# Performance work log

Hardware: AMD Instinct MI355X
Metric: run time of the kernel (lower is better)

## Reference

```python
import jax, jax.numpy as jnp
import numpy as np

K = 10
A_JAC = 0.5
B_JAC = 0.5
N_NODES = 100000
N_EDGES = 1600000
IN_CH, HID, OUT_CH = 256, 64, 32
NUM_LAYERS = 2


def setup_inputs() -> dict:
    key = jax.random.key(0)
    k1, k2, k3, k4, k5, k6 = jax.random.split(key, 6)
    x = jax.random.normal(k1, (N_NODES, IN_CH), dtype=jnp.float32)
    edge_index = jax.random.randint(k2, (2, N_EDGES), 0, N_NODES, dtype=jnp.int64)
    W1 = jax.random.normal(k3, (IN_CH, HID), dtype=jnp.float32) / np.sqrt(IN_CH)
    b1 = jnp.zeros((HID,), dtype=jnp.float32)
    coeffs = jnp.ones((NUM_LAYERS, K + 1), dtype=jnp.float32) / (K + 1)
    W2 = jax.random.normal(k4, (HID, OUT_CH), dtype=jnp.float32) / np.sqrt(HID)
    b2 = jnp.zeros((OUT_CH,), dtype=jnp.float32)
    return {"x": x, "edge_index": edge_index, "W1": W1, "b1": b1,
            "coeffs": coeffs, "W2": W2, "b2": b2}


def _build_norm(edge_index, num_nodes):
    # add self loops (as PyG add_self_loops does)
    loops = jnp.arange(num_nodes, dtype=edge_index.dtype)
    row = jnp.concatenate([edge_index[0], loops])
    col = jnp.concatenate([edge_index[1], loops])
    deg = jax.ops.segment_sum(jnp.ones_like(col, dtype=jnp.float32), col,
                              num_segments=num_nodes)
    dinv = jnp.where(deg > 0, deg ** -0.5, 0.0)
    norm = dinv[row] * dinv[col]  # [E + N]
    return row, col, norm


def _propagate(h, row, col, norm, num_nodes):
    # out[i] = sum_{e: col[e]=i} norm[e] * h[row[e]]
    return jax.ops.segment_sum(norm[:, None] * h[row], col, num_segments=num_nodes)


def _jacobi_conv(h, row, col, norm, c, num_nodes):
    a, b = A_JAC, B_JAC
    Tx0 = h
    out = c[0] * Tx0
    Tx1 = _propagate(h, row, col, norm, num_nodes)
    out = out + c[1] * Tx1
    for k in range(2, K + 1):
        n = k - 1
        A_n = (2 * n + a + b + 1) * (2 * n + a + b + 2) / (2 * (n + 1) * (n + a + b + 1))
        B_n = (a ** 2 - b ** 2) * (2 * n + a + b + 1) / (2 * (n + 1) * (n + a + b + 1) * (2 * n + a + b))
        C_n = (n + a) * (n + b) * (2 * n + a + b + 2) / ((n + 1) * (n + a + b + 1) * (2 * n + a + b))
        Tx2 = A_n * _propagate(Tx1, row, col, norm, num_nodes) + B_n * Tx1 - C_n * Tx0
        out = out + c[k] * Tx2
        Tx0, Tx1 = Tx1, Tx2
    return out


def reference(x, edge_index, W1, b1, coeffs, W2, b2):
    num_nodes = x.shape[0]
    row, col, norm = _build_norm(edge_index, num_nodes)
    h = jax.nn.relu(x @ W1 + b1)
    for l in range(NUM_LAYERS):
        h = jax.nn.relu(_jacobi_conv(h, row, col, norm, coeffs[l], num_nodes))
    return h @ W2 + b2
```

## Files before the change

kernel.cpp:

```cpp
#include <hip/hip_runtime.h>
#include <hip/hip_fp16.h>

#define NN 100000
#define NE 1600000
#define KORD 10
#define HID 64

#define NBUK ((NN + 255) / 256)
#define BCAP 8192
#define EPB  (NE / 256)

typedef _Float16 half8v __attribute__((ext_vector_type(8)));
typedef _Float16 half4v __attribute__((ext_vector_type(4)));
typedef float float4v __attribute__((ext_vector_type(4)));

__device__ __forceinline__ float2 up2(unsigned u) {
    __half2 hh = *(__half2*)&u;
    return __half22float2(hh);
}
__device__ __forceinline__ unsigned pk2(float a, float b) {
    __half2 hh = __floats2half2_rn(a, b);
    return *(unsigned*)&hh;
}

__global__ __launch_bounds__(512) void k_zero(int* __restrict__ gcnt,
                                              int* __restrict__ dhist) {
    int t = threadIdx.x;
    if (t < NBUK) gcnt[t] = 0;
    if (t < 64) dhist[t] = 0;
}

__global__ __launch_bounds__(1024) void k_binA(const int* __restrict__ ei,
                                               int* __restrict__ gcnt,
                                               unsigned* __restrict__ staged) {
    __shared__ int lh[NBUK];
    __shared__ int lcur[NBUK];
    int t = threadIdx.x;
    int ebeg = blockIdx.x * EPB;
    int eend = min(ebeg + EPB, NE);
    for (int i = t; i < NBUK; i += 1024) lh[i] = 0;
    __syncthreads();
    for (int e = ebeg + t; e < eend; e += 1024)
        atomicAdd(&lh[ei[NE + e] >> 8], 1);
    __syncthreads();
    for (int i = t; i < NBUK; i += 1024)
        lcur[i] = lh[i] ? atomicAdd(&gcnt[i], lh[i]) : 0;
    __syncthreads();
    for (int e = ebeg + t; e < eend; e += 1024) {
        int r = ei[e], c = ei[NE + e];
        int bkt = c >> 8;
        int slot = atomicAdd(&lcur[bkt], 1);
        if (slot < BCAP)
            staged[(size_t)bkt * BCAP + slot] = ((unsigned)(c & 255) << 24) | (unsigned)r;
    }
}

__global__ __launch_bounds__(512) void k_bscan(const int* __restrict__ gcnt,
                                               int* __restrict__ bbase,
                                               int* __restrict__ cursor) {
    __shared__ int tmp[512];
    int t = threadIdx.x;
    int v = (t < NBUK) ? gcnt[t] : 0;
    tmp[t] = v;
    __syncthreads();
    int x = v;
    for (int off = 1; off < 512; off <<= 1) {
        int y = (t >= off) ? tmp[t - off] : 0;
        __syncthreads();
        x += y;
        tmp[t] = x;
        __syncthreads();
    }
    if (t < NBUK) bbase[t] = x - v;
    if (t == 0) cursor[NN] = NE;
}

__global__ __launch_bounds__(512) void k_binB(const unsigned* __restrict__ staged,
                                              const int* __restrict__ gcnt,
                                              const int* __restrict__ bbase,
                                              int* __restrict__ cursor,
                                              int* __restrict__ cnt,
                                              float* __restrict__ dinv,
                                              int* __restrict__ csr) {
    __shared__ unsigned lrec[BCAP];
    __shared__ int lcnt[256], lcur[256], ltmp[256];
    int b = blockIdx.x, t = threadIdx.x;
    int count = min(gcnt[b], BCAP);
    int base = bbase[b];
    if (t < 256) lcnt[t] = 0;
    __syncthreads();
    for (int i = t; i < count; i += 512) {
        unsigned rec = staged[(size_t)b * BCAP + i];
        lrec[i] = rec;
        atomicAdd(&lcnt[rec >> 24], 1);
    }
    __syncthreads();
    int v = 0, x = 0;
    if (t < 256) { v = lcnt[t]; ltmp[t] = v; }
    __syncthreads();
    x = v;
    for (int off = 1; off < 256; off <<= 1) {
        int y = (t < 256 && t >= off) ? ltmp[t - off] : 0;
        __syncthreads();
        if (t < 256) { x += y; ltmp[t] = x; }
        __syncthreads();
    }
    if (t < 256) {
        int excl = x - v;
        lcur[t] = base + excl;
        int node = b * 256 + t;
        if (node < NN) {
            cursor[node] = base + excl;
            cnt[node] = v;
            dinv[node] = rsqrtf((float)(v + 1));
        }
    }
    __syncthreads();
    for (int i = t; i < count; i += 512) {
        unsigned rec = lrec[i];
        int pos = atomicAdd(&lcur[rec >> 24], 1);
        csr[pos] = (int)(rec & 0xFFFFFFu);
    }
}

__global__ __launch_bounds__(256) void k_dhist(const int* __restrict__ cnt,
                                               int* __restrict__ dhist) {
    __shared__ int lh[64];
    int t = threadIdx.x;
    if (t < 64) lh[t] = 0;
    __syncthreads();
    int i = blockIdx.x * 256 + t;
    if (i < NN) atomicAdd(&lh[min(cnt[i], 63)], 1);
    __syncthreads();
    if (t < 64 && lh[t]) atomicAdd(&dhist[t], lh[t]);
}

__global__ void k_dscan(int* __restrict__ dhist) {
    __shared__ int tmp[64];
    int t = threadIdx.x;
    int v = dhist[t];
    tmp[t] = v;
    __syncthreads();
    int x = v;
    for (int off = 1; off < 64; off <<= 1) {
        int y = (t >= off) ? tmp[t - off] : 0;
        __syncthreads();
        x += y;
        tmp[t] = x;
        __syncthreads();
    }
    dhist[t] = x - v;
}

__global__ __launch_bounds__(256) void k_dperm(const int* __restrict__ cnt,
                                               int* __restrict__ dhist,
                                               int* __restrict__ perm) {
    __shared__ int lh[64], lb[64];
    int t = threadIdx.x;
    if (t < 64) lh[t] = 0;
    __syncthreads();
    int i = blockIdx.x * 256 + t;
    int b = 0, my = 0;
    if (i < NN) { b = min(cnt[i], 63); my = atomicAdd(&lh[b], 1); }
    __syncthreads();
    if (t < 64) lb[t] = lh[t] ? atomicAdd(&dhist[t], lh[t]) : 0;
    __syncthreads();
    if (i < NN) perm[lb[b] + my] = i;
}

__global__ __launch_bounds__(256) void k_zrow(__half* __restrict__ a, __half* __restrict__ b,
                                              __half* __restrict__ c, __half* __restrict__ d) {
    int t = threadIdx.x;
    __half z = __float2half(0.f);
    size_t base = (size_t)NN * HID;
    if (t < 64)       a[base + t] = z;
    else if (t < 128) b[base + (t - 64)] = z;
    else if (t < 192) c[base + (t - 128)] = z;
    else              d[base + (t - 192)] = z;
}

__global__ __launch_bounds__(256) void k_prepw1(const float* __restrict__ W1,
                                                _Float16* __restrict__ W1T) {
    int f = blockIdx.x * 256 + threadIdx.x;
    int n = f >> 8, k = f & 255;
    W1T[f] = (_Float16)W1[k * 64 + n];
}

#define G1K 128
#define G1S 136
__global__ __launch_bounds__(256) void k_gemm1(const float* __restrict__ x,
                                               const _Float16* __restrict__ W1T,
                                               const float* __restrict__ b1,
                                               const float* __restrict__ dinv,
                                               __half* __restrict__ h) {
    __shared__ _Float16 A_lds[64 * G1S];
    __shared__ _Float16 B_lds[64 * G1S];
    int t = threadIdx.x;
    int wave = t >> 6, lane = t & 63;
    int quad = lane >> 4, m16 = lane & 15;
    int row0 = blockIdx.x * 64;

    float4v acc[4];
#pragma unroll
    for (int n4 = 0; n4 < 4; ++n4) acc[n4] = (float4v){0.f, 0.f, 0.f, 0.f};

    for (int c = 0; c < 2; ++c) {
        int k0 = c * G1K;
#pragma unroll
        for (int i = 0; i < 8; ++i) {
            int f = i * 256 + t;
            int r = f >> 5, c4 = f & 31;
            int grow = row0 + r;
            float4 v = (grow < NN) ? *(const float4*)&x[(size_t)grow * 256 + k0 + c4 * 4]
                                   : make_float4(0.f, 0.f, 0.f, 0.f);
            half4v hv = {(_Float16)v.x, (_Float16)v.y, (_Float16)v.z, (_Float16)v.w};
            *(half4v*)&A_lds[r * G1S + c4 * 4] = hv;
        }
#pragma unroll
        for (int i = 0; i < 4; ++i) {
            int f = i * 256 + t;
            int n = f >> 4, k8 = f & 15;
            *(half8v*)&B_lds[n * G1S + k8 * 8] =
                *(const half8v*)&W1T[n * 256 + k0 + k8 * 8];
        }
        __syncthreads();

#pragma unroll
        for (int s = 0; s < 4; ++s) {
            half8v af = *(const half8v*)&A_lds[(wave * 16 + m16) * G1S + s * 32 + quad * 8];
#pragma unroll
            for (int n4 = 0; n4 < 4; ++n4) {
                half8v bf = *(const half8v*)&B_lds[(n4 * 16 + m16) * G1S + s * 32 + quad * 8];
                acc[n4] = __builtin_amdgcn_mfma_f32_16x16x32_f16(af, bf, acc[n4], 0, 0, 0);
            }
        }
        __syncthreads();
    }

    float bv[4];
#pragma unroll
    for (int n4 = 0; n4 < 4; ++n4) bv[n4] = b1[n4 * 16 + m16];
#pragma unroll
    for (int r = 0; r < 4; ++r) {
        int grow = row0 + wave * 16 + quad * 4 + r;
        if (grow >= NN) continue;
        float dv = dinv[grow];
#pragma unroll
        for (int n4 = 0; n4 < 4; ++n4) {
            float v = dv * fmaxf(acc[n4][r] + bv[n4], 0.f);
            h[(size_t)grow * 64 + n4 * 16 + m16] = __float2half(v);
        }
    }
}

__global__ __launch_bounds__(256) void k_prop(const int* __restrict__ cursor,
                                              const int* __restrict__ csr,
                                              const int* __restrict__ perm,
                                              const __half* __restrict__ src,
                                              const __half* __restrict__ t0,
                                              const float* __restrict__ dinv,
                                              __half* __restrict__ dst,
                                              __half* __restrict__ acc,
                                              __half* __restrict__ hout,
                                              float An, float Bn, float Cn,
                                              const float* __restrict__ coeffs,
                                              int cbase, int kidx, int init,
                                              int finalize, int unscale) {
    int slot = ((blockIdx.x * 256 + threadIdx.x) >> 6) * 8 + ((threadIdx.x & 63) >> 3);
    int ch8 = (threadIdx.x & 7) * 8;
    bool valid = slot < NN;
    int node = valid ? perm[slot] : 0;
    int beg = valid ? cursor[node] : 0;
    int end = valid ? cursor[node + 1] : 0;

    int len = end - beg;
    int q = len >> 2;
    int j0 = beg,          e0 = beg + q;
    int j1 = e0,           e1 = beg + 2 * q;
    int j2 = e1,           e2 = beg + 3 * q;
    int j3 = e2,           e3 = end;

    float p[8];
#pragma unroll
    for (int i = 0; i < 8; ++i) p[i] = 0.f;

    while (__any(j3 < e3)) {
        int a0 = (j0 < e0) ? j0 : 0;
        int a1 = (j1 < e1) ? j1 : 0;
        int a2 = (j2 < e2) ? j2 : 0;
        int a3 = (j3 < e3) ? j3 : 0;
        int v0 = csr[a0], v1 = csr[a1], v2 = csr[a2], v3 = csr[a3];
        int r0 = (j0 < e0) ? v0 : NN;
        int r1 = (j1 < e1) ? v1 : NN;
        int r2 = (j2 < e2) ? v2 : NN;
        int r3 = (j3 < e3) ? v3 : NN;
        uint4 u0 = *(const uint4*)&src[(size_t)r0 * HID + ch8];
        uint4 u1 = *(const uint4*)&src[(size_t)r1 * HID + ch8];
        uint4 u2 = *(const uint4*)&src[(size_t)r2 * HID + ch8];
        uint4 u3 = *(const uint4*)&src[(size_t)r3 * HID + ch8];
        {
            float2 f0 = up2(u0.x), f1 = up2(u0.y), f2 = up2(u0.z), f3 = up2(u0.w);
            p[0] += f0.x; p[1] += f0.y; p[2] += f1.x; p[3] += f1.y;
            p[4] += f2.x; p[5] += f2.y; p[6] += f3.x; p[7] += f3.y;
        }
        {
            float2 f0 = up2(u1.x), f1 = up2(u1.y), f2 = up2(u1.z), f3 = up2(u1.w);
            p[0] += f0.x; p[1] += f0.y; p[2] += f1.x; p[3] += f1.y;
            p[4] += f2.x; p[5] += f2.y; p[6] += f3.x; p[7] += f3.y;
        }
        {
            float2 f0 = up2(u2.x), f1 = up2(u2.y), f2 = up2(u2.z), f3 = up2(u2.w);
            p[0] += f0.x; p[1] += f0.y; p[2] += f1.x; p[3] += f1.y;
            p[4] += f2.x; p[5] += f2.y; p[6] += f3.x; p[7] += f3.y;
        }
        {
            float2 f0 = up2(u3.x), f1 = up2(u3.y), f2 = up2(u3.z), f3 = up2(u3.w);
            p[0] += f0.x; p[1] += f0.y; p[2] += f1.x; p[3] += f1.y;
            p[4] += f2.x; p[5] += f2.y; p[6] += f3.x; p[7] += f3.y;
        }
        ++j0; ++j1; ++j2; ++j3;
    }

    if (!valid) return;
    size_t idx = (size_t)node * HID + ch8;
    float dv = dinv[node];
    float dv2 = dv * dv;

    uint4 sr = *(const uint4*)&src[idx];
    float2 s01 = up2(sr.x), s23 = up2(sr.y), s45 = up2(sr.z), s67 = up2(sr.w);
    float sv[8] = {s01.x, s01.y, s23.x, s23.y, s45.x, s45.y, s67.x, s67.y};

    uint4 tr = *(const uint4*)&t0[idx];
    float2 t01 = up2(tr.x), t23 = up2(tr.y), t45 = up2(tr.z), t67 = up2(tr.w);
    float tv[8] = {t01.x, t01.y, t23.x, t23.y, t45.x, t45.y, t67.x, t67.y};

    float v[8];
#pragma unroll
    for (int i = 0; i < 8; ++i)
        v[i] = An * dv2 * (p[i] + sv[i]) + Bn * sv[i] - Cn * tv[i];

    if (!finalize) {
        uint4 o;
        o.x = pk2(v[0], v[1]); o.y = pk2(v[2], v[3]);
        o.z = pk2(v[4], v[5]); o.w = pk2(v[6], v[7]);
        *(uint4*)&dst[idx] = o;
    }

    float ck = coeffs[cbase + kidx];
    float av[8];
    if (init) {
        float c0 = coeffs[cbase];
#pragma unroll
        for (int i = 0; i < 8; ++i) av[i] = c0 * sv[i];
    } else {
        uint4 ar = *(const uint4*)&acc[idx];
        float2 a01 = up2(ar.x), a23 = up2(ar.y), a45 = up2(ar.z), a67 = up2(ar.w);
        av[0] = a01.x; av[1] = a01.y; av[2] = a23.x; av[3] = a23.y;
        av[4] = a45.x; av[5] = a45.y; av[6] = a67.x; av[7] = a67.y;
    }
#pragma unroll
    for (int i = 0; i < 8; ++i) av[i] += ck * v[i];

    uint4 o;
    if (finalize) {
        float s = unscale ? (1.0f / dv) : 1.0f;
        o.x = pk2(s * fmaxf(av[0], 0.f), s * fmaxf(av[1], 0.f));
        o.y = pk2(s * fmaxf(av[2], 0.f), s * fmaxf(av[3], 0.f));
        o.z = pk2(s * fmaxf(av[4], 0.f), s * fmaxf(av[5], 0.f));
        o.w = pk2(s * fmaxf(av[6], 0.f), s * fmaxf(av[7], 0.f));
        *(uint4*)&hout[idx] = o;
    } else {
        o.x = pk2(av[0], av[1]); o.y = pk2(av[2], av[3]);
        o.z = pk2(av[4], av[5]); o.w = pk2(av[6], av[7]);
        *(uint4*)&acc[idx] = o;
    }
}

__global__ __launch_bounds__(256) void k_gemm2(const __half* __restrict__ h,
                                               const float* __restrict__ W2,
                                               const float* __restrict__ b2,
                                               float* __restrict__ out) {
    __shared__ float W2s[64 * 32];
    __shared__ float b2s[32];
    int t = threadIdx.x;
    for (int i = t * 4; i < 64 * 32; i += 256 * 4)
        *(float4*)&W2s[i] = *(const float4*)&W2[i];
    if (t < 32) b2s[t] = b2[t];
    __syncthreads();

    int gid = blockIdx.x * 256 + t;
    int row = gid >> 3;
    int c4 = (t & 7) * 4;
    if (row >= NN) return;
    const __half* hr = h + (size_t)row * 64;
    float4 acc = *(const float4*)&b2s[c4];
#pragma unroll
    for (int k8 = 0; k8 < 8; ++k8) {
        uint4 raw = *(const uint4*)&hr[k8 * 8];
        float2 a01 = up2(raw.x), a23 = up2(raw.y), a45 = up2(raw.z), a67 = up2(raw.w);
        float a[8] = {a01.x, a01.y, a23.x, a23.y, a45.x, a45.y, a67.x, a67.y};
#pragma unroll
        for (int j = 0; j < 8; ++j) {
            float4 w = *(const float4*)&W2s[(k8 * 8 + j) * 32 + c4];
            acc.x += a[j] * w.x;
            acc.y += a[j] * w.y;
            acc.z += a[j] * w.z;
            acc.w += a[j] * w.w;
        }
    }
    *(float4*)&out[(size_t)row * 32 + c4] = acc;
}

extern "C" void kernel_launch(void* const* d_in, const int* in_sizes, int n_in,
                              void* d_out, int out_size, void* d_ws, size_t ws_size,
                              hipStream_t stream) {
    const float* x      = (const float*)d_in[0];
    const int*   ei     = (const int*)d_in[1];
    const float* W1     = (const float*)d_in[2];
    const float* b1     = (const float*)d_in[3];
    const float* coeffs = (const float*)d_in[4];
    const float* W2     = (const float*)d_in[5];
    const float* b2     = (const float*)d_in[6];
    float* out = (float*)d_out;

    char* ws = (char*)d_ws;
    size_t off = 0;
    auto alloc = [&](size_t bytes) { void* p = ws + off; off += (bytes + 255) & ~(size_t)255; return p; };
    int*      cnt    = (int*)alloc(NN * 4);
    int*      cursor = (int*)alloc((NN + 1) * 4);
    float*    dinv   = (float*)alloc(NN * 4);
    int*      csr    = (int*)alloc((size_t)NE * 4);
    int*      dhist  = (int*)alloc(64 * 4);
    int*      perm   = (int*)alloc(NN * 4);
    int*      gcnt   = (int*)alloc(NBUK * 4);
    int*      bbase  = (int*)alloc(NBUK * 4);
    unsigned* staged = (unsigned*)alloc((size_t)NBUK * BCAP * 4);
    _Float16* W1T    = (_Float16*)alloc(256 * 64 * 2);
    __half*   h16    = (__half*)alloc((size_t)(NN + 1) * HID * 2);
    __half*   bufA   = (__half*)alloc((size_t)(NN + 1) * HID * 2);
    __half*   bufB   = (__half*)alloc((size_t)(NN + 1) * HID * 2);
    __half*   bufC   = (__half*)alloc((size_t)(NN + 1) * HID * 2);
    __half*   accb   = (__half*)alloc((size_t)NN * HID * 2);

    const int BN = (NN + 255) / 256;
    const int BP = (NN + 31) / 32;

    k_zero<<<1, 512, 0, stream>>>(gcnt, dhist);
    k_binA<<<256, 1024, 0, stream>>>(ei, gcnt, staged);
    k_bscan<<<1, 512, 0, stream>>>(gcnt, bbase, cursor);
    k_binB<<<NBUK, 512, 0, stream>>>(staged, gcnt, bbase, cursor, cnt, dinv, csr);

    k_dhist<<<BN, 256, 0, stream>>>(cnt, dhist);
    k_dscan<<<1, 64, 0, stream>>>(dhist);
    k_dperm<<<BN, 256, 0, stream>>>(cnt, dhist, perm);
    k_zrow<<<1, 256, 0, stream>>>(h16, bufA, bufB, bufC);

    k_prepw1<<<64, 256, 0, stream>>>(W1, W1T);
    k_gemm1<<<(NN + 63) / 64, 256, 0, stream>>>(x, W1T, b1, dinv, h16);

    __half* rot[4] = {h16, bufA, bufB, bufC};

    for (int l = 0; l < 2; ++l) {
        int cbase = l * (KORD + 1);
        k_prop<<<BP, 256, 0, stream>>>(cursor, csr, perm, rot[0], rot[0], dinv,
                                       rot[1], accb, h16, 1.0f, 0.0f, 0.0f,
                                       coeffs, cbase, 1, 1, 0, 0);
        for (int k = 2; k <= KORD; ++k) {
            __half* dst = rot[k & 3];
            const __half* s1 = rot[(k - 1) & 3];
            const __half* s0 = rot[(k - 2) & 3];
            double n = k - 1, a = 0.5, b = 0.5;
            double An = (2*n + a + b + 1) * (2*n + a + b + 2) / (2 * (n + 1) * (n + a + b + 1));
            double Bn = (a*a - b*b) * (2*n + a + b + 1) / (2 * (n + 1) * (n + a + b + 1) * (2*n + a + b));
            double Cn = (n + a) * (n + b) * (2*n + a + b + 2) / ((n + 1) * (n + a + b + 1) * (2*n + a + b));
            k_prop<<<BP, 256, 0, stream>>>(cursor, csr, perm, s1, s0, dinv,
                                           dst, accb, h16, (float)An, (float)Bn, (float)Cn,
                                           coeffs, cbase, k, 0,
                                           (k == KORD) ? 1 : 0, l);
        }
    }

    k_gemm2<<<(NN * 8 + 255) / 256, 256, 0, stream>>>(h16, W2, b2, out);
}
```

Baseline: 1.040 ms.

## Pad CSR neighbor lists to multiples of eight for vectorized gather loop

Each node's neighbor list is padded to a multiple of eight entries using the zero row index NN. Segments are now allocated with a global atomic instead of a separate bucket scan kernel, and each node stores (start, iters) in place of cursor pairs. The propagation loop reads neighbor indices as two int4 loads and issues eight independent row gathers per iteration with no per-lane bounds checks. The cost is up to seven extra dummy gathers per node, a larger CSR buffer, and a CSR order that depends on atomic allocation.

```diff
diff --git a/kernel.cpp b/kernel.cpp
--- a/kernel.cpp
+++ b/kernel.cpp
@@ -9,6 +9,7 @@
 #define NBUK ((NN + 255) / 256)
 #define BCAP 8192
 #define EPB  (NE / 256)
+#define CSR_CAP (NE + 8 * NN)
 
 typedef _Float16 half8v __attribute__((ext_vector_type(8)));
 typedef _Float16 half4v __attribute__((ext_vector_type(4)));
@@ -24,10 +25,12 @@
 }
 
 __global__ __launch_bounds__(512) void k_zero(int* __restrict__ gcnt,
-                                              int* __restrict__ dhist) {
+                                              int* __restrict__ dhist,
+                                              int* __restrict__ palloc) {
     int t = threadIdx.x;
     if (t < NBUK) gcnt[t] = 0;
     if (t < 64) dhist[t] = 0;
+    if (t == 511) *palloc = 0;
 }
 
 __global__ __launch_bounds__(1024) void k_binA(const int* __restrict__ ei,
@@ -55,38 +58,18 @@
     }
 }
 
-__global__ __launch_bounds__(512) void k_bscan(const int* __restrict__ gcnt,
-                                               int* __restrict__ bbase,
-                                               int* __restrict__ cursor) {
-    __shared__ int tmp[512];
-    int t = threadIdx.x;
-    int v = (t < NBUK) ? gcnt[t] : 0;
-    tmp[t] = v;
-    __syncthreads();
-    int x = v;
-    for (int off = 1; off < 512; off <<= 1) {
-        int y = (t >= off) ? tmp[t - off] : 0;
-        __syncthreads();
-        x += y;
-        tmp[t] = x;
-        __syncthreads();
-    }
-    if (t < NBUK) bbase[t] = x - v;
-    if (t == 0) cursor[NN] = NE;
-}
-
 __global__ __launch_bounds__(512) void k_binB(const unsigned* __restrict__ staged,
                                               const int* __restrict__ gcnt,
-                                              const int* __restrict__ bbase,
-                                              int* __restrict__ cursor,
+                                              int* __restrict__ palloc,
                                               int* __restrict__ cnt,
                                               float* __restrict__ dinv,
-                                              int* __restrict__ csr) {
+                                              int* __restrict__ csr,
+                                              int2* __restrict__ seg) {
     __shared__ unsigned lrec[BCAP];
     __shared__ int lcnt[256], lcur[256], ltmp[256];
+    __shared__ int lbase;
     int b = blockIdx.x, t = threadIdx.x;
     int count = min(gcnt[b], BCAP);
-    int base = bbase[b];
     if (t < 256) lcnt[t] = 0;
     __syncthreads();
     for (int i = t; i < count; i += 512) {
@@ -95,24 +78,28 @@
         atomicAdd(&lcnt[rec >> 24], 1);
     }
     __syncthreads();
-    int v = 0, x = 0;
-    if (t < 256) { v = lcnt[t]; ltmp[t] = v; }
-    __syncthreads();
-    x = v;
+    int v = 0, plen = 0;
+    if (t < 256) { v = lcnt[t]; plen = (v + 7) & ~7; ltmp[t] = plen; }
+    __syncthreads();
+    int x = plen;
     for (int off = 1; off < 256; off <<= 1) {
         int y = (t < 256 && t >= off) ? ltmp[t - off] : 0;
         __syncthreads();
         if (t < 256) { x += y; ltmp[t] = x; }
         __syncthreads();
     }
+    if (t == 255) lbase = atomicAdd(palloc, x);
+    __syncthreads();
+    int start = 0;
     if (t < 256) {
-        int excl = x - v;
-        lcur[t] = base + excl;
+        start = lbase + x - plen;
+        lcur[t] = start;
         int node = b * 256 + t;
         if (node < NN) {
-            cursor[node] = base + excl;
             cnt[node] = v;
             dinv[node] = rsqrtf((float)(v + 1));
+            seg[node] = make_int2(start, plen >> 3);
+            for (int i = v; i < plen; ++i) csr[start + i] = NN;
         }
     }
     __syncthreads();
@@ -253,7 +240,11 @@
     }
 }
 
-__global__ __launch_bounds__(256) void k_prop(const int* __restrict__ cursor,
+#define ACC8(u) { float2 f0 = up2((u).x), f1 = up2((u).y), f2 = up2((u).z), f3 = up2((u).w); \
+    p[0] += f0.x; p[1] += f0.y; p[2] += f1.x; p[3] += f1.y; \
+    p[4] += f2.x; p[5] += f2.y; p[6] += f3.x; p[7] += f3.y; }
+
+__global__ __launch_bounds__(256) void k_prop(const int2* __restrict__ seg,
                                               const int* __restrict__ csr,
                                               const int* __restrict__ perm,
                                               const __half* __restrict__ src,
@@ -270,55 +261,27 @@
     int ch8 = (threadIdx.x & 7) * 8;
     bool valid = slot < NN;
     int node = valid ? perm[slot] : 0;
-    int beg = valid ? cursor[node] : 0;
-    int end = valid ? cursor[node + 1] : 0;
-
-    int len = end - beg;
-    int q = len >> 2;
-    int j0 = beg,          e0 = beg + q;
-    int j1 = e0,           e1 = beg + 2 * q;
-    int j2 = e1,           e2 = beg + 3 * q;
-    int j3 = e2,           e3 = end;
+    int2 sg = valid ? seg[node] : make_int2(0, 0);
+    const int4* cp = (const int4*)(csr + sg.x);
+    int iters = sg.y;
 
     float p[8];
 #pragma unroll
     for (int i = 0; i < 8; ++i) p[i] = 0.f;
 
-    while (__any(j3 < e3)) {
-        int a0 = (j0 < e0) ? j0 : 0;
-        int a1 = (j1 < e1) ? j1 : 0;
-        int a2 = (j2 < e2) ? j2 : 0;
-        int a3 = (j3 < e3) ? j3 : 0;
-        int v0 = csr[a0], v1 = csr[a1], v2 = csr[a2], v3 = csr[a3];
-        int r0 = (j0 < e0) ? v0 : NN;
-        int r1 = (j1 < e1) ? v1 : NN;
-        int r2 = (j2 < e2) ? v2 : NN;
-        int r3 = (j3 < e3) ? v3 : NN;
-        uint4 u0 = *(const uint4*)&src[(size_t)r0 * HID + ch8];
-        uint4 u1 = *(const uint4*)&src[(size_t)r1 * HID + ch8];
-        uint4 u2 = *(const uint4*)&src[(size_t)r2 * HID + ch8];
-        uint4 u3 = *(const uint4*)&src[(size_t)r3 * HID + ch8];
-        {
-            float2 f0 = up2(u0.x), f1 = up2(u0.y), f2 = up2(u0.z), f3 = up2(u0.w);
-            p[0] += f0.x; p[1] += f0.y; p[2] += f1.x; p[3] += f1.y;
-            p[4] += f2.x; p[5] += f2.y; p[6] += f3.x; p[7] += f3.y;
-        }
-        {
-            float2 f0 = up2(u1.x), f1 = up2(u1.y), f2 = up2(u1.z), f3 = up2(u1.w);
-            p[0] += f0.x; p[1] += f0.y; p[2] += f1.x; p[3] += f1.y;
-            p[4] += f2.x; p[5] += f2.y; p[6] += f3.x; p[7] += f3.y;
-        }
-        {
-            float2 f0 = up2(u2.x), f1 = up2(u2.y), f2 = up2(u2.z), f3 = up2(u2.w);
-            p[0] += f0.x; p[1] += f0.y; p[2] += f1.x; p[3] += f1.y;
-            p[4] += f2.x; p[5] += f2.y; p[6] += f3.x; p[7] += f3.y;
-        }
-        {
-            float2 f0 = up2(u3.x), f1 = up2(u3.y), f2 = up2(u3.z), f3 = up2(u3.w);
-            p[0] += f0.x; p[1] += f0.y; p[2] += f1.x; p[3] += f1.y;
-            p[4] += f2.x; p[5] += f2.y; p[6] += f3.x; p[7] += f3.y;
-        }
-        ++j0; ++j1; ++j2; ++j3;
+    for (int it = 0; it < iters; ++it) {
+        int4 ia = cp[it * 2];
+        int4 ib = cp[it * 2 + 1];
+        uint4 u0 = *(const uint4*)&src[(size_t)ia.x * HID + ch8];
+        uint4 u1 = *(const uint4*)&src[(size_t)ia.y * HID + ch8];
+        uint4 u2 = *(const uint4*)&src[(size_t)ia.z * HID + ch8];
+        uint4 u3 = *(const uint4*)&src[(size_t)ia.w * HID + ch8];
+        uint4 u4 = *(const uint4*)&src[(size_t)ib.x * HID + ch8];
+        uint4 u5 = *(const uint4*)&src[(size_t)ib.y * HID + ch8];
+        uint4 u6 = *(const uint4*)&src[(size_t)ib.z * HID + ch8];
+        uint4 u7 = *(const uint4*)&src[(size_t)ib.w * HID + ch8];
+        ACC8(u0); ACC8(u1); ACC8(u2); ACC8(u3);
+        ACC8(u4); ACC8(u5); ACC8(u6); ACC8(u7);
     }
 
     if (!valid) return;
@@ -427,13 +390,13 @@
     size_t off = 0;
     auto alloc = [&](size_t bytes) { void* p = ws + off; off += (bytes + 255) & ~(size_t)255; return p; };
     int*      cnt    = (int*)alloc(NN * 4);
-    int*      cursor = (int*)alloc((NN + 1) * 4);
     float*    dinv   = (float*)alloc(NN * 4);
-    int*      csr    = (int*)alloc((size_t)NE * 4);
+    int*      csr    = (int*)alloc((size_t)CSR_CAP * 4);
+    int2*     seg    = (int2*)alloc((size_t)NN * 8);
     int*      dhist  = (int*)alloc(64 * 4);
     int*      perm   = (int*)alloc(NN * 4);
     int*      gcnt   = (int*)alloc(NBUK * 4);
-    int*      bbase  = (int*)alloc(NBUK * 4);
+    int*      palloc = (int*)alloc(4);
     unsigned* staged = (unsigned*)alloc((size_t)NBUK * BCAP * 4);
     _Float16* W1T    = (_Float16*)alloc(256 * 64 * 2);
     __half*   h16    = (__half*)alloc((size_t)(NN + 1) * HID * 2);
@@ -445,10 +408,9 @@
     const int BN = (NN + 255) / 256;
     const int BP = (NN + 31) / 32;
 
-    k_zero<<<1, 512, 0, stream>>>(gcnt, dhist);
+    k_zero<<<1, 512, 0, stream>>>(gcnt, dhist, palloc);
     k_binA<<<256, 1024, 0, stream>>>(ei, gcnt, staged);
-    k_bscan<<<1, 512, 0, stream>>>(gcnt, bbase, cursor);
-    k_binB<<<NBUK, 512, 0, stream>>>(staged, gcnt, bbase, cursor, cnt, dinv, csr);
+    k_binB<<<NBUK, 512, 0, stream>>>(staged, gcnt, palloc, cnt, dinv, csr, seg);
 
     k_dhist<<<BN, 256, 0, stream>>>(cnt, dhist);
     k_dscan<<<1, 64, 0, stream>>>(dhist);
@@ -462,7 +424,7 @@
 
     for (int l = 0; l < 2; ++l) {
         int cbase = l * (KORD + 1);
-        k_prop<<<BP, 256, 0, stream>>>(cursor, csr, perm, rot[0], rot[0], dinv,
+        k_prop<<<BP, 256, 0, stream>>>(seg, csr, perm, rot[0], rot[0], dinv,
                                        rot[1], accb, h16, 1.0f, 0.0f, 0.0f,
                                        coeffs, cbase, 1, 1, 0, 0);
         for (int k = 2; k <= KORD; ++k) {
@@ -473,7 +435,7 @@
             double An = (2*n + a + b + 1) * (2*n + a + b + 2) / (2 * (n + 1) * (n + a + b + 1));
             double Bn = (a*a - b*b) * (2*n + a + b + 1) / (2 * (n + 1) * (n + a + b + 1) * (2*n + a + b));
             double Cn = (n + a) * (n + b) * (2*n + a + b + 2) / ((n + 1) * (n + a + b + 1) * (2*n + a + b));
-            k_prop<<<BP, 256, 0, stream>>>(cursor, csr, perm, s1, s0, dinv,
+            k_prop<<<BP, 256, 0, stream>>>(seg, csr, perm, s1, s0, dinv,
                                            dst, accb, h16, (float)An, (float)Bn, (float)Cn,
                                            coeffs, cbase, k, 0,
                                            (k == KORD) ? 1 : 0, l);
```

After: 995.0 us. 1.04x faster.
